# Optimization experiments

Measured on AMD Instinct MI355X. Metric: run time of the kernel, lower is better.

The kernel has to match this reference:

```python
import jax, jax.numpy as jnp
import numpy as np

N = 4096
IN_F = 256
OUT_F = 64
HEADS = 4
NEG_SLOPE = 0.2


def setup_inputs() -> dict:
    key = jax.random.key(0)
    k1, k2, k3, k4 = jax.random.split(key, 4)
    x = jax.random.normal(k1, (N, IN_F), dtype=jnp.float32)
    W = jax.random.normal(k2, (HEADS, IN_F, OUT_F), dtype=jnp.float32) * (1.0 / np.sqrt(IN_F))
    a = jax.random.normal(k3, (HEADS, 2 * OUT_F), dtype=jnp.float32) * (1.0 / np.sqrt(2 * OUT_F))
    adj_matrix = jax.random.randint(k4, (N, N), 0, 2, dtype=jnp.int32)
    return {"x": x, "W": W, "a": a, "adj_matrix": adj_matrix}


def reference(x, W, a, adj_matrix):
    heads, in_f, out_f = W.shape
    n = x.shape[0]
    # per-head linear transform: [H, N, F]
    xt = jnp.einsum('ni,hio->hno', x, W)
    # attention logit decomposes: a . cat(xt_i, xt_j) = src_i + dst_j
    src = jnp.einsum('hnf,hf->hn', xt, a[:, :out_f])   # [H, N]
    dst = jnp.einsum('hnf,hf->hn', xt, a[:, out_f:])   # [H, N]
    e = jax.nn.leaky_relu(src[:, :, None] + dst[:, None, :], NEG_SLOPE)  # [H, N, N]
    mask = (adj_matrix > 0)[None, :, :]
    e = jnp.where(mask, e, -jnp.inf)
    attention = jax.nn.softmax(e, axis=2)              # [H, N, N]
    # (dropout is identity in eval / p=0)
    h_prime = jnp.einsum('hij,hjf->hif', attention, xt)  # [H, N, F]
    # concat heads: [N, H*F]
    return h_prime.transpose(1, 0, 2).reshape(n, heads * out_f)
```

## Files before the change

### kernel.cpp

```cpp
#include <hip/hip_runtime.h>
#include <math.h>

#define N 4096
#define IN_F 256
#define OUT_F 64
#define HEADS 4
#define NEG 0.2f
#define JLEN 512
#define NC (JLEN / 32)
#define LOG2E 1.44269504088896f
#define RSTR 68

typedef float f32x4 __attribute__((ext_vector_type(4)));
typedef float f32x2 __attribute__((ext_vector_type(2)));
typedef short short8 __attribute__((ext_vector_type(8)));

#define FMA4S(A, s, V) do { (A).x = fmaf((s),(V).x,(A).x); (A).y = fmaf((s),(V).y,(A).y); \
                            (A).z = fmaf((s),(V).z,(A).z); (A).w = fmaf((s),(V).w,(A).w); } while(0)

#define MSEL(P, MS, R) (P) = __uint_as_float(__float_as_uint(P) & \
                         (unsigned)__builtin_amdgcn_sbfe((int)(MS), (R), 1))

__device__ __forceinline__ unsigned short f2bf(float x) {
  unsigned int u = __float_as_uint(x);
  u += 0x7fffu + ((u >> 16) & 1u);
  return (unsigned short)(u >> 16);
}

__device__ __forceinline__ float exp2_fast(float x) {
#if __has_builtin(__builtin_amdgcn_exp2f)
  return __builtin_amdgcn_exp2f(x);
#else
  return exp2f(x);
#endif
}

__device__ __forceinline__ int cvt_pk_bf16(float lo, float hi) {
  int r;
  asm("v_cvt_pk_bf16_f32 %0, %1, %2" : "=v"(r) : "v"(lo), "v"(hi));
  return r;
}

__global__ __launch_bounds__(256) void k_prep(const float* __restrict__ x,
                                              const float* __restrict__ W,
                                              const float* __restrict__ a,
                                              const int* __restrict__ adj,
                                              short* __restrict__ xtB,
                                              float* __restrict__ src,
                                              float* __restrict__ dst,
                                              unsigned char* __restrict__ mbB) {
  __shared__ __align__(16) float xls[32 * 68];
  __shared__ __align__(16) float wls[64 * 64];
  const int t = threadIdx.x;

  if (blockIdx.x >= 512) {
    int tid = (blockIdx.x - 512) * 256 + t;
    const int4* a4 = (const int4*)adj + (size_t)tid * 2;
    int4 v0 = a4[0];
    int4 v1 = a4[1];
    unsigned b = 0;
    b |= (v0.x > 0) ? 0x01u : 0u;
    b |= (v0.y > 0) ? 0x02u : 0u;
    b |= (v0.z > 0) ? 0x04u : 0u;
    b |= (v0.w > 0) ? 0x08u : 0u;
    b |= (v1.x > 0) ? 0x10u : 0u;
    b |= (v1.y > 0) ? 0x20u : 0u;
    b |= (v1.z > 0) ? 0x40u : 0u;
    b |= (v1.w > 0) ? 0x80u : 0u;
    mbB[tid] = (unsigned char)b;
    return;
  }

  const int h  = blockIdx.x >> 7;
  const int bx = blockIdx.x & 127;
  const int i0 = bx * 32;
  const int fg = t & 15;
  const int rg = t >> 4;

  float4 acc[2];
  acc[0] = acc[1] = make_float4(0.f, 0.f, 0.f, 0.f);

  const float4* xg = (const float4*)x;
  const float4* wg = (const float4*)W;
  float4* xls4 = (float4*)xls;
  float4* wls4 = (float4*)wls;
  const float4* xr4 = (const float4*)xls;
  const float4* wr4 = (const float4*)wls;

  for (int kt = 0; kt < 4; ++kt) {
    __syncthreads();
    #pragma unroll
    for (int s = 0; s < 2; ++s) {
      int f4i = t + 256 * s;
      int row = f4i >> 4, c4 = f4i & 15;
      xls4[row * 17 + c4] = xg[(size_t)(i0 + row) * 64 + kt * 16 + c4];
    }
    #pragma unroll
    for (int s = 0; s < 4; ++s) {
      int f4i = t + 256 * s;
      int kk = f4i >> 4, c4 = f4i & 15;
      wls4[kk * 16 + c4] = wg[(size_t)(h * 256 + kt * 64 + kk) * 16 + c4];
    }
    __syncthreads();
    #pragma unroll 4
    for (int kk = 0; kk < 64; kk += 4) {
      float4 wv0 = wr4[(kk + 0) * 16 + fg];
      float4 wv1 = wr4[(kk + 1) * 16 + fg];
      float4 wv2 = wr4[(kk + 2) * 16 + fg];
      float4 wv3 = wr4[(kk + 3) * 16 + fg];
      #pragma unroll
      for (int q = 0; q < 2; ++q) {
        float4 xv = xr4[(rg * 2 + q) * 17 + (kk >> 2)];
        FMA4S(acc[q], xv.x, wv0);
        FMA4S(acc[q], xv.y, wv1);
        FMA4S(acc[q], xv.z, wv2);
        FMA4S(acc[q], xv.w, wv3);
      }
    }
  }

  const float4* a4 = (const float4*)a;
  float4 as = a4[h * 32 + fg];
  float4 ad = a4[h * 32 + 16 + fg];
  as.x *= LOG2E; as.y *= LOG2E; as.z *= LOG2E; as.w *= LOG2E;
  ad.x *= LOG2E; ad.y *= LOG2E; ad.z *= LOG2E; ad.w *= LOG2E;
  #pragma unroll
  for (int q = 0; q < 2; ++q) {
    float s_ = acc[q].x * as.x + acc[q].y * as.y + acc[q].z * as.z + acc[q].w * as.w;
    float d_ = acc[q].x * ad.x + acc[q].y * ad.y + acc[q].z * ad.z + acc[q].w * ad.w;
    #pragma unroll
    for (int off = 1; off < 16; off <<= 1) {
      s_ += __shfl_xor(s_, off, 64);
      d_ += __shfl_xor(d_, off, 64);
    }
    if (fg == 0) {
      int r = rg * 2 + q;
      src[h * N + i0 + r] = s_;
      dst[h * N + i0 + r] = d_;
    }
  }

  __syncthreads();
  #pragma unroll
  for (int q = 0; q < 2; ++q) {
    *(float4*)&xls[(rg * 2 + q) * 68 + fg * 4] = acc[q];
  }
  __syncthreads();

  {
    const int lane = t & 63;
    const int g    = t >> 6;
    const int q    = lane >> 4;
    const int m    = lane & 15;
    short8 bv;
    #pragma unroll
    for (int r = 0; r < 8; ++r) {
      bv[r] = (short)f2bf(xls[(q * 8 + r) * 68 + g * 16 + m]);
    }
    ((short8*)xtB)[((size_t)(h * 128 + bx) * 4 + g) * 64 + lane] = bv;
  }
}

__global__ __launch_bounds__(512) void k_flash(const unsigned* __restrict__ mb,
                                               const float* __restrict__ src,
                                               const float* __restrict__ dst,
                                               const short* __restrict__ xtB,
                                               float* __restrict__ out) {
  __shared__ __align__(16) float smem[4 * 32 * RSTR];
  const int t    = threadIdx.x;
  const int lane = t & 63;
  const int w    = t >> 6;
  const int h    = blockIdx.y;
  const int i0   = blockIdx.x * 32;
  const int q    = lane >> 4;
  const int m    = lane & 15;
  const int koff = q * 8;
  const int jbase = w * JLEN;

  {
    const float4* dg = (const float4*)(dst + (size_t)h * N);
    float4* ds4 = (float4*)smem;
    ds4[t]       = dg[t];
    ds4[t + 512] = dg[t + 512];
  }

  float sv = (lane < 32) ? src[h * N + i0 + lane] : 0.f;
  const float s0 = __shfl(sv, m, 64);
  const float s1 = __shfl(sv, 16 + m, 64);
  __syncthreads();

  f32x4 acc0[4], acc1[4], accL0, accL1;
  #pragma unroll
  for (int g = 0; g < 4; ++g) { acc0[g] = (f32x4)(0.f); acc1[g] = (f32x4)(0.f); }
  accL0 = (f32x4)(0.f);
  accL1 = (f32x4)(0.f);

  short8 ones;
  #pragma unroll
  for (int r = 0; r < 8; ++r) ones[r] = (short)0x3F80;

  const f32x2 s02 = (f32x2)(s0);
  const f32x2 s12 = (f32x2)(s1);

  const unsigned* mrow0 = mb + (size_t)(i0 + m) * 128 + w * NC;
  const unsigned* mrow1 = mb + (size_t)(i0 + 16 + m) * 128 + w * NC;
  const short8* xbb = (const short8*)xtB + ((size_t)(h * 128 + w * NC) * 4) * 64 + lane;

#define LOADC(DM0, DM1, DB, CIDX) do {                                     \
    DM0 = mrow0[CIDX];                                                     \
    DM1 = mrow1[CIDX];                                                     \
    const short8* bb_ = xbb + (size_t)(CIDX) * 256;                        \
    DB[0] = bb_[0]; DB[1] = bb_[64]; DB[2] = bb_[128]; DB[3] = bb_[192];   \
  } while (0)

#define COMPUTE(CM0, CM1, CB, C) do {                                      \
    const float* dp_ = &smem[jbase + (C) * 32 + koff];                     \
    union { float4 v[2]; f32x2 h2[4]; float f[8]; } du;                    \
    du.v[0] = *(const float4*)dp_;                                         \
    du.v[1] = *(const float4*)(dp_ + 4);                                   \
    unsigned ms0 = (CM0) >> koff;                                          \
    unsigned ms1 = (CM1) >> koff;                                          \
    int av0[4], av1[4];                                                    \
    _Pragma("unroll")                                                      \
    for (int r2 = 0; r2 < 4; ++r2) {                                       \
      f32x2 d2 = du.h2[r2];                                                \
      f32x2 e0 = s02 + d2;                                                 \
      f32x2 el0 = __builtin_elementwise_max(e0, e0 * NEG);                 \
      f32x2 e1 = s12 + d2;                                                 \
      f32x2 el1 = __builtin_elementwise_max(e1, e1 * NEG);                 \
      float p0a = exp2_fast(el0.x), p0b = exp2_fast(el0.y);                \
      float p1a = exp2_fast(el1.x), p1b = exp2_fast(el1.y);                \
      MSEL(p0a, ms0, 2 * r2);  MSEL(p0b, ms0, 2 * r2 + 1);                 \
      MSEL(p1a, ms1, 2 * r2);  MSEL(p1b, ms1, 2 * r2 + 1);                 \
      av0[r2] = cvt_pk_bf16(p0a, p0b);                                     \
      av1[r2] = cvt_pk_bf16(p1a, p1b);                                     \
    }                                                                      \
    short8 af0 = __builtin_bit_cast(short8, *(int4*)av0);                  \
    short8 af1 = __builtin_bit_cast(short8, *(int4*)av1);                  \
    acc0[0] = __builtin_amdgcn_mfma_f32_16x16x32_bf16(af0, CB[0], acc0[0], 0, 0, 0); \
    acc0[1] = __builtin_amdgcn_mfma_f32_16x16x32_bf16(af0, CB[1], acc0[1], 0, 0, 0); \
    acc0[2] = __builtin_amdgcn_mfma_f32_16x16x32_bf16(af0, CB[2], acc0[2], 0, 0, 0); \
    acc0[3] = __builtin_amdgcn_mfma_f32_16x16x32_bf16(af0, CB[3], acc0[3], 0, 0, 0); \
    accL0   = __builtin_amdgcn_mfma_f32_16x16x32_bf16(af0, ones,  accL0,   0, 0, 0); \
    acc1[0] = __builtin_amdgcn_mfma_f32_16x16x32_bf16(af1, CB[0], acc1[0], 0, 0, 0); \
    acc1[1] = __builtin_amdgcn_mfma_f32_16x16x32_bf16(af1, CB[1], acc1[1], 0, 0, 0); \
    acc1[2] = __builtin_amdgcn_mfma_f32_16x16x32_bf16(af1, CB[2], acc1[2], 0, 0, 0); \
    acc1[3] = __builtin_amdgcn_mfma_f32_16x16x32_bf16(af1, CB[3], acc1[3], 0, 0, 0); \
    accL1   = __builtin_amdgcn_mfma_f32_16x16x32_bf16(af1, ones,  accL1,   0, 0, 0); \
  } while (0)

  unsigned cM0, cM1, nM0, nM1;
  short8 cB[4], nB[4];
  LOADC(cM0, cM1, cB, 0);

  for (int c = 0; c < NC; ++c) {
    const int cn = (c + 1 < NC) ? c + 1 : c;
    LOADC(nM0, nM1, nB, cn);

    COMPUTE(cM0, cM1, cB, c);

    cM0 = nM0; cM1 = nM1;
    #pragma unroll
    for (int z = 0; z < 4; ++z) cB[z] = nB[z];
  }
#undef LOADC
#undef COMPUTE

#define RED_ST(SLOT) do {                                                  \
    float* part_ = smem + (SLOT) * (32 * RSTR);                            \
    _Pragma("unroll")                                                      \
    for (int g = 0; g < 4; ++g)                                            \
      _Pragma("unroll")                                                    \
      for (int rr = 0; rr < 4; ++rr) {                                     \
        part_[(q * 4 + rr) * RSTR + g * 16 + m]      = acc0[g][rr];        \
        part_[(q * 4 + rr + 16) * RSTR + g * 16 + m] = acc1[g][rr];        \
      }                                                                    \
    if (m == 0) {                                                          \
      _Pragma("unroll")                                                    \
      for (int rr = 0; rr < 4; ++rr) {                                     \
        part_[(q * 4 + rr) * RSTR + 64]      = accL0[rr];                  \
        part_[(q * 4 + rr + 16) * RSTR + 64] = accL1[rr];                  \
      }                                                                    \
    }                                                                      \
  } while (0)
#define RED_ADD(SLOT) do {                                                 \
    const float* part_ = smem + (SLOT) * (32 * RSTR);                      \
    _Pragma("unroll")                                                      \
    for (int g = 0; g < 4; ++g)                                            \
      _Pragma("unroll")                                                    \
      for (int rr = 0; rr < 4; ++rr) {                                     \
        acc0[g][rr] += part_[(q * 4 + rr) * RSTR + g * 16 + m];            \
        acc1[g][rr] += part_[(q * 4 + rr + 16) * RSTR + g * 16 + m];       \
      }                                                                    \
    _Pragma("unroll")                                                      \
    for (int rr = 0; rr < 4; ++rr) {                                       \
      accL0[rr] += part_[(q * 4 + rr) * RSTR + 64];                        \
      accL1[rr] += part_[(q * 4 + rr + 16) * RSTR + 64];                   \
    }                                                                      \
  } while (0)

  __syncthreads();
  if (w >= 4) RED_ST(w - 4);
  __syncthreads();
  if (w < 4) { RED_ADD(w); RED_ST(w); }
  __syncthreads();
#undef RED_ST
#undef RED_ADD

  {
    const int row = t >> 4;
    const int c4  = t & 15;
    const float* p = smem + row * RSTR + c4 * 4;
    const float* pl = smem + row * RSTR + 64;
    float4 v = *(const float4*)p;
    float l = pl[0];
    #pragma unroll
    for (int slot = 1; slot < 4; ++slot) {
      const float4 u = *(const float4*)(p + slot * (32 * RSTR));
      v.x += u.x; v.y += u.y; v.z += u.z; v.w += u.w;
      l += pl[slot * (32 * RSTR)];
    }
    const float il = 1.f / l;
    v.x *= il; v.y *= il; v.z *= il; v.w *= il;
    ((float4*)out)[(size_t)(i0 + row) * 64 + h * 16 + c4] = v;
  }
}

extern "C" void kernel_launch(void* const* d_in, const int* in_sizes, int n_in,
                              void* d_out, int out_size, void* d_ws, size_t ws_size,
                              hipStream_t stream) {
  const float* x   = (const float*)d_in[0];
  const float* W   = (const float*)d_in[1];
  const float* a   = (const float*)d_in[2];
  const int*   adj = (const int*)d_in[3];
  float* out = (float*)d_out;

  float* ws    = (float*)d_ws;
  short* xtB   = (short*)ws;
  float* src   = ws + 524288;
  float* dst   = src + HEADS * N;
  unsigned* mb = (unsigned*)(dst + HEADS * N);

  k_prep<<<dim3(512 + N * N / 8 / 256), 256, 0, stream>>>(x, W, a, adj, xtB, src, dst,
                                                          (unsigned char*)mb);
  k_flash<<<dim3(N / 32, HEADS), 512, 0, stream>>>(mb, src, dst, xtB, out);
}
```

Measured before the change: 134.2 us.

## Fuse adjacency mask packing into attention kernel, processing two heads per block

Removes the separate mask-packing pass from the prep kernel. The flash kernel now reads the int32 adjacency matrix directly and compacts it to bitmasks through per-wave LDS nibble staging. Each block handles two heads with four j-slices per head and double-buffered loads, and the bf16 pack uses a perm-based rounding instead of the cvt instruction. This trades a separate pass and the mask write/read for reading the 64 MB adjacency twice inside the compute kernel, and it assumes adjacency values are exactly 0 or 1.

```diff
diff --git a/kernel.cpp b/kernel.cpp
--- a/kernel.cpp
+++ b/kernel.cpp
@@ -6,8 +6,8 @@
 #define OUT_F 64
 #define HEADS 4
 #define NEG 0.2f
-#define JLEN 512
-#define NC (JLEN / 32)
+#define JSL 1024
+#define NC2 (JSL / 32)
 #define LOG2E 1.44269504088896f
 #define RSTR 68
 
@@ -35,41 +35,21 @@
 #endif
 }
 
-__device__ __forceinline__ int cvt_pk_bf16(float lo, float hi) {
-  int r;
-  asm("v_cvt_pk_bf16_f32 %0, %1, %2" : "=v"(r) : "v"(lo), "v"(hi));
-  return r;
+__device__ __forceinline__ int pack_bf2(float p0, float p1) {
+  unsigned u0 = __float_as_uint(p0) + 0x8000u;
+  unsigned u1 = __float_as_uint(p1) + 0x8000u;
+  return (int)__builtin_amdgcn_perm(u1, u0, 0x07060302u);
 }
 
 __global__ __launch_bounds__(256) void k_prep(const float* __restrict__ x,
                                               const float* __restrict__ W,
                                               const float* __restrict__ a,
-                                              const int* __restrict__ adj,
                                               short* __restrict__ xtB,
                                               float* __restrict__ src,
-                                              float* __restrict__ dst,
-                                              unsigned char* __restrict__ mbB) {
+                                              float* __restrict__ dst) {
   __shared__ __align__(16) float xls[32 * 68];
   __shared__ __align__(16) float wls[64 * 64];
   const int t = threadIdx.x;
-
-  if (blockIdx.x >= 512) {
-    int tid = (blockIdx.x - 512) * 256 + t;
-    const int4* a4 = (const int4*)adj + (size_t)tid * 2;
-    int4 v0 = a4[0];
-    int4 v1 = a4[1];
-    unsigned b = 0;
-    b |= (v0.x > 0) ? 0x01u : 0u;
-    b |= (v0.y > 0) ? 0x02u : 0u;
-    b |= (v0.z > 0) ? 0x04u : 0u;
-    b |= (v0.w > 0) ? 0x08u : 0u;
-    b |= (v1.x > 0) ? 0x10u : 0u;
-    b |= (v1.y > 0) ? 0x20u : 0u;
-    b |= (v1.z > 0) ? 0x40u : 0u;
-    b |= (v1.w > 0) ? 0x80u : 0u;
-    mbB[tid] = (unsigned char)b;
-    return;
-  }
 
   const int h  = blockIdx.x >> 7;
   const int bx = blockIdx.x & 127;
@@ -161,27 +141,33 @@
   }
 }
 
-__global__ __launch_bounds__(512) void k_flash(const unsigned* __restrict__ mb,
-                                               const float* __restrict__ src,
-                                               const float* __restrict__ dst,
-                                               const short* __restrict__ xtB,
-                                               float* __restrict__ out) {
+__global__ __launch_bounds__(512, 2) void k_flash(const int* __restrict__ adj,
+                                                  const float* __restrict__ src,
+                                                  const float* __restrict__ dst,
+                                                  const short* __restrict__ xtB,
+                                                  float* __restrict__ out) {
   __shared__ __align__(16) float smem[4 * 32 * RSTR];
   const int t    = threadIdx.x;
   const int lane = t & 63;
   const int w    = t >> 6;
-  const int h    = blockIdx.y;
+  const int hb   = blockIdx.y;
   const int i0   = blockIdx.x * 32;
+  const int hh   = w >> 2;
+  const int sl   = w & 3;
+  const int h    = hb * 2 + hh;
+  const int jbase = sl * JSL;
   const int q    = lane >> 4;
   const int m    = lane & 15;
   const int koff = q * 8;
-  const int jbase = w * JLEN;
 
   {
-    const float4* dg = (const float4*)(dst + (size_t)h * N);
+    const float4* dgA = (const float4*)(dst + (size_t)(hb * 2) * N);
+    const float4* dgB = (const float4*)(dst + (size_t)(hb * 2 + 1) * N);
     float4* ds4 = (float4*)smem;
-    ds4[t]       = dg[t];
-    ds4[t + 512] = dg[t + 512];
+    ds4[t]        = dgA[t];
+    ds4[t + 512]  = dgA[t + 512];
+    ds4[t + 1024] = dgB[t];
+    ds4[t + 1536] = dgB[t + 512];
   }
 
   float sv = (lane < 32) ? src[h * N + i0 + lane] : 0.f;
@@ -202,24 +188,49 @@
   const f32x2 s02 = (f32x2)(s0);
   const f32x2 s12 = (f32x2)(s1);
 
-  const unsigned* mrow0 = mb + (size_t)(i0 + m) * 128 + w * NC;
-  const unsigned* mrow1 = mb + (size_t)(i0 + 16 + m) * 128 + w * NC;
-  const short8* xbb = (const short8*)xtB + ((size_t)(h * 128 + w * NC) * 4) * 64 + lane;
-
-#define LOADC(DM0, DM1, DB, CIDX) do {                                     \
-    DM0 = mrow0[CIDX];                                                     \
-    DM1 = mrow1[CIDX];                                                     \
+  char* nib = (char*)smem + 32768 + w * 256;
+  const int nboff = (lane >> 3) * 8 + (lane & 7);
+  const char* nibr = nib + m * 8;
+
+  const int4* apb = (const int4*)adj;
+  const size_t a0 = (size_t)(i0 + (lane >> 3)) * 1024 + (size_t)(jbase >> 2) + (lane & 7);
+
+  const short8* xbb = (const short8*)xtB + ((size_t)(h * 128 + (jbase >> 5)) * 4) * 64 + lane;
+
+#define LOADC(AJ, DB, CIDX) do {                                           \
+    AJ[0] = apb[a0 +         (size_t)(CIDX) * 8];                          \
+    AJ[1] = apb[a0 +  8192 + (size_t)(CIDX) * 8];                          \
+    AJ[2] = apb[a0 + 16384 + (size_t)(CIDX) * 8];                          \
+    AJ[3] = apb[a0 + 24576 + (size_t)(CIDX) * 8];                          \
     const short8* bb_ = xbb + (size_t)(CIDX) * 256;                        \
     DB[0] = bb_[0]; DB[1] = bb_[64]; DB[2] = bb_[128]; DB[3] = bb_[192];   \
   } while (0)
 
-#define COMPUTE(CM0, CM1, CB, C) do {                                      \
-    const float* dp_ = &smem[jbase + (C) * 32 + koff];                     \
+#define NIBCOMP(R64, MW) do {                                              \
+    unsigned lo_ = (unsigned)(R64), hi_ = (unsigned)((R64) >> 32);         \
+    lo_ = (lo_ | (lo_ >> 4)) & 0x00ff00ffu;                                \
+    lo_ = (lo_ | (lo_ >> 8)) & 0x0000ffffu;                                \
+    hi_ = (hi_ | (hi_ >> 4)) & 0x00ff00ffu;                                \
+    hi_ = (hi_ | (hi_ >> 8)) & 0x0000ffffu;                                \
+    MW  = lo_ | (hi_ << 16);                                               \
+  } while (0)
+
+#define COMPUTE(AJ, DB, C) do {                                            \
+    nib[  0 + nboff] = (char)(AJ[0].x | (AJ[0].y << 1) | (AJ[0].z << 2) | (AJ[0].w << 3)); \
+    nib[ 64 + nboff] = (char)(AJ[1].x | (AJ[1].y << 1) | (AJ[1].z << 2) | (AJ[1].w << 3)); \
+    nib[128 + nboff] = (char)(AJ[2].x | (AJ[2].y << 1) | (AJ[2].z << 2) | (AJ[2].w << 3)); \
+    nib[192 + nboff] = (char)(AJ[3].x | (AJ[3].y << 1) | (AJ[3].z << 2) | (AJ[3].w << 3)); \
+    unsigned long long r0_ = *(const unsigned long long*)(nibr);           \
+    unsigned long long r1_ = *(const unsigned long long*)(nibr + 128);     \
+    unsigned cM0, cM1;                                                     \
+    NIBCOMP(r0_, cM0);                                                     \
+    NIBCOMP(r1_, cM1);                                                     \
+    const float* dp_ = &smem[hh * 4096 + jbase + (C) * 32 + koff];         \
     union { float4 v[2]; f32x2 h2[4]; float f[8]; } du;                    \
     du.v[0] = *(const float4*)dp_;                                         \
     du.v[1] = *(const float4*)(dp_ + 4);                                   \
-    unsigned ms0 = (CM0) >> koff;                                          \
-    unsigned ms1 = (CM1) >> koff;                                          \
+    unsigned ms0 = cM0 >> koff;                                            \
+    unsigned ms1 = cM1 >> koff;                                            \
     int av0[4], av1[4];                                                    \
     _Pragma("unroll")                                                      \
     for (int r2 = 0; r2 < 4; ++r2) {                                       \
@@ -232,38 +243,36 @@
       float p1a = exp2_fast(el1.x), p1b = exp2_fast(el1.y);                \
       MSEL(p0a, ms0, 2 * r2);  MSEL(p0b, ms0, 2 * r2 + 1);                 \
       MSEL(p1a, ms1, 2 * r2);  MSEL(p1b, ms1, 2 * r2 + 1);                 \
-      av0[r2] = cvt_pk_bf16(p0a, p0b);                                     \
-      av1[r2] = cvt_pk_bf16(p1a, p1b);                                     \
+      av0[r2] = pack_bf2(p0a, p0b);                                        \
+      av1[r2] = pack_bf2(p1a, p1b);                                        \
     }                                                                      \
     short8 af0 = __builtin_bit_cast(short8, *(int4*)av0);                  \
     short8 af1 = __builtin_bit_cast(short8, *(int4*)av1);                  \
-    acc0[0] = __builtin_amdgcn_mfma_f32_16x16x32_bf16(af0, CB[0], acc0[0], 0, 0, 0); \
-    acc0[1] = __builtin_amdgcn_mfma_f32_16x16x32_bf16(af0, CB[1], acc0[1], 0, 0, 0); \
-    acc0[2] = __builtin_amdgcn_mfma_f32_16x16x32_bf16(af0, CB[2], acc0[2], 0, 0, 0); \
-    acc0[3] = __builtin_amdgcn_mfma_f32_16x16x32_bf16(af0, CB[3], acc0[3], 0, 0, 0); \
+    acc0[0] = __builtin_amdgcn_mfma_f32_16x16x32_bf16(af0, DB[0], acc0[0], 0, 0, 0); \
+    acc0[1] = __builtin_amdgcn_mfma_f32_16x16x32_bf16(af0, DB[1], acc0[1], 0, 0, 0); \
+    acc0[2] = __builtin_amdgcn_mfma_f32_16x16x32_bf16(af0, DB[2], acc0[2], 0, 0, 0); \
+    acc0[3] = __builtin_amdgcn_mfma_f32_16x16x32_bf16(af0, DB[3], acc0[3], 0, 0, 0); \
     accL0   = __builtin_amdgcn_mfma_f32_16x16x32_bf16(af0, ones,  accL0,   0, 0, 0); \
-    acc1[0] = __builtin_amdgcn_mfma_f32_16x16x32_bf16(af1, CB[0], acc1[0], 0, 0, 0); \
-    acc1[1] = __builtin_amdgcn_mfma_f32_16x16x32_bf16(af1, CB[1], acc1[1], 0, 0, 0); \
-    acc1[2] = __builtin_amdgcn_mfma_f32_16x16x32_bf16(af1, CB[2], acc1[2], 0, 0, 0); \
-    acc1[3] = __builtin_amdgcn_mfma_f32_16x16x32_bf16(af1, CB[3], acc1[3], 0, 0, 0); \
+    acc1[0] = __builtin_amdgcn_mfma_f32_16x16x32_bf16(af1, DB[0], acc1[0], 0, 0, 0); \
+    acc1[1] = __builtin_amdgcn_mfma_f32_16x16x32_bf16(af1, DB[1], acc1[1], 0, 0, 0); \
+    acc1[2] = __builtin_amdgcn_mfma_f32_16x16x32_bf16(af1, DB[2], acc1[2], 0, 0, 0); \
+    acc1[3] = __builtin_amdgcn_mfma_f32_16x16x32_bf16(af1, DB[3], acc1[3], 0, 0, 0); \
     accL1   = __builtin_amdgcn_mfma_f32_16x16x32_bf16(af1, ones,  accL1,   0, 0, 0); \
   } while (0)
 
-  unsigned cM0, cM1, nM0, nM1;
-  short8 cB[4], nB[4];
-  LOADC(cM0, cM1, cB, 0);
-
-  for (int c = 0; c < NC; ++c) {
-    const int cn = (c + 1 < NC) ? c + 1 : c;
-    LOADC(nM0, nM1, nB, cn);
-
-    COMPUTE(cM0, cM1, cB, c);
-
-    cM0 = nM0; cM1 = nM1;
-    #pragma unroll
-    for (int z = 0; z < 4; ++z) cB[z] = nB[z];
+  int4 AJ0[4], AJ1[4];
+  short8 B0[4], B1[4];
+  LOADC(AJ0, B0, 0);
+  LOADC(AJ1, B1, 1);
+
+  for (int c = 0; c < NC2; c += 2) {
+    COMPUTE(AJ0, B0, c);
+    { const int cn = (c + 2 < NC2) ? c + 2 : c; LOADC(AJ0, B0, cn); }
+    COMPUTE(AJ1, B1, c + 1);
+    { const int cn = (c + 3 < NC2) ? c + 3 : c + 1; LOADC(AJ1, B1, cn); }
   }
 #undef LOADC
+#undef NIBCOMP
 #undef COMPUTE
 
 #define RED_ST(SLOT) do {                                                  \
@@ -300,29 +309,31 @@
   } while (0)
 
   __syncthreads();
-  if (w >= 4) RED_ST(w - 4);
-  __syncthreads();
-  if (w < 4) { RED_ADD(w); RED_ST(w); }
+  if (sl >= 2) RED_ST(hh * 2 + (sl - 2));
+  __syncthreads();
+  if (sl < 2) { RED_ADD(hh * 2 + sl); RED_ST(hh * 2 + sl); }
   __syncthreads();
 #undef RED_ST
 #undef RED_ADD
 
   {
-    const int row = t >> 4;
-    const int c4  = t & 15;
-    const float* p = smem + row * RSTR + c4 * 4;
-    const float* pl = smem + row * RSTR + 64;
-    float4 v = *(const float4*)p;
-    float l = pl[0];
-    #pragma unroll
-    for (int slot = 1; slot < 4; ++slot) {
-      const float4 u = *(const float4*)(p + slot * (32 * RSTR));
-      v.x += u.x; v.y += u.y; v.z += u.z; v.w += u.w;
-      l += pl[slot * (32 * RSTR)];
-    }
-    const float il = 1.f / l;
-    v.x *= il; v.y *= il; v.z *= il; v.w *= il;
-    ((float4*)out)[(size_t)(i0 + row) * 64 + h * 16 + c4] = v;
+    const int hf  = t >> 8;
+    const int row = (t >> 3) & 31;
+    const int c8  = t & 7;
+    const float* pA = smem + (hf * 2)     * (32 * RSTR) + row * RSTR;
+    const float* pB = smem + (hf * 2 + 1) * (32 * RSTR) + row * RSTR;
+    const float il = 1.f / (pA[64] + pB[64]);
+    float4 v0 = *(const float4*)(pA + c8 * 8);
+    float4 u0 = *(const float4*)(pB + c8 * 8);
+    float4 v1 = *(const float4*)(pA + c8 * 8 + 4);
+    float4 u1 = *(const float4*)(pB + c8 * 8 + 4);
+    v0.x = (v0.x + u0.x) * il; v0.y = (v0.y + u0.y) * il;
+    v0.z = (v0.z + u0.z) * il; v0.w = (v0.w + u0.w) * il;
+    v1.x = (v1.x + u1.x) * il; v1.y = (v1.y + u1.y) * il;
+    v1.z = (v1.z + u1.z) * il; v1.w = (v1.w + u1.w) * il;
+    float4* og = (float4*)out + (size_t)(i0 + row) * 64 + (hb * 2 + hf) * 16 + c8 * 2;
+    og[0] = v0;
+    og[1] = v1;
   }
 }
 
@@ -339,9 +350,7 @@
   short* xtB   = (short*)ws;
   float* src   = ws + 524288;
   float* dst   = src + HEADS * N;
-  unsigned* mb = (unsigned*)(dst + HEADS * N);
-
-  k_prep<<<dim3(512 + N * N / 8 / 256), 256, 0, stream>>>(x, W, a, adj, xtB, src, dst,
-                                                          (unsigned char*)mb);
-  k_flash<<<dim3(N / 32, HEADS), 512, 0, stream>>>(mb, src, dst, xtB, out);
-}
+
+  k_prep<<<dim3(512), 256, 0, stream>>>(x, W, a, xtB, src, dst);
+  k_flash<<<dim3(N / 32, 2), 512, 0, stream>>>(adj, src, dst, xtB, out);
+}
```

Measured after the change: 157.2 us. 17.1% more time.
